# Performance work log

Measured on AMD Instinct MI355X. Metric: run time of the kernel, lower is better.

The kernel has to match this reference:

```python
import jax, jax.numpy as jnp
import numpy as np

EPS = 1e-5

def _layernorm(x, gamma, beta):
    mu = jnp.mean(x, axis=-1, keepdims=True)
    var = jnp.mean(jnp.square(x - mu), axis=-1, keepdims=True)
    return (x - mu) * jax.lax.rsqrt(var + EPS) * gamma + beta

def setup_inputs() -> dict:
    key = jax.random.key(0)
    ks = jax.random.split(key, 8)
    B, T, H = 8, 4096, 512
    s = 1.0 / np.sqrt(H)  # torch LSTM init scale
    return {
        "x": jax.random.normal(ks[0], (B, T, H), jnp.float32),
        "W_ih": jax.random.uniform(ks[1], (4 * H, H), jnp.float32, -s, s),
        "W_hh": jax.random.uniform(ks[2], (4 * H, H), jnp.float32, -s, s),
        "b_ih": jax.random.uniform(ks[3], (4 * H,), jnp.float32, -s, s),
        "b_hh": jax.random.uniform(ks[4], (4 * H,), jnp.float32, -s, s),
        "gamma": jnp.ones((H,), jnp.float32),
        "beta": jnp.zeros((H,), jnp.float32),
        "W_lin": jax.random.uniform(ks[5], (H, H), jnp.float32, -s, s),
        "b_lin": jax.random.uniform(ks[6], (H,), jnp.float32, -s, s),
    }

def _lstm(res, W_ih, W_hh, b_ih, b_hh):
    # res: [B, T, H]; torch gate order: i, f, g, o
    B, T, H = res.shape
    # precompute input contributions for all timesteps: [T, B, 4H]
    x_proj = jnp.einsum('bth,gh->tbg', res, W_ih) + (b_ih + b_hh)

    def step(carry, xp):
        h, c = carry  # [B, H] each
        gates = xp + h @ W_hh.T  # [B, 4H]
        i, f, g, o = jnp.split(gates, 4, axis=-1)
        i = jax.nn.sigmoid(i)
        f = jax.nn.sigmoid(f)
        g = jnp.tanh(g)
        o = jax.nn.sigmoid(o)
        c = f * c + i * g
        h = o * jnp.tanh(c)
        return (h, c), h

    h0 = jnp.zeros((B, H), res.dtype)
    c0 = jnp.zeros((B, H), res.dtype)
    (hT, cT), hs = jax.lax.scan(step, (h0, c0), x_proj)
    out = jnp.transpose(hs, (1, 0, 2))  # [B, T, H]
    return out, (hT[None], cT[None])

def reference(x, W_ih, W_hh, b_ih, b_hh, gamma, beta, W_lin, b_lin):
    res = _layernorm(x, gamma, beta)
    out, out_state = _lstm(res, W_ih, W_hh, b_ih, b_hh)
    gate = jax.nn.silu(res @ W_lin.T + b_lin)
    out = out * gate + res
    return (out, out_state)
```

## Files before the change

### kernel.cpp

```cpp
#include <hip/hip_runtime.h>
#include <math.h>

#define NB 8
#define HID 512

typedef unsigned int uint4v __attribute__((ext_vector_type(4)));

__device__ __forceinline__ float sigf(float x) { return 1.0f / (1.0f + __expf(-x)); }
__device__ __forceinline__ float tanhf_(float x) {
    return 2.0f / (1.0f + __expf(-2.0f * x)) - 1.0f;
}

__global__ void init_ws_kernel(unsigned long long* h_bufs) {
    h_bufs[blockIdx.x * 256 + threadIdx.x] = 0ull;
}

__global__ void ln_kernel(const float* __restrict__ x, const float* __restrict__ gamma,
                          const float* __restrict__ beta, float* __restrict__ res,
                          int t0, int chsh) {
    int wid = threadIdx.x >> 6, lane = threadIdx.x & 63;
    int rl = blockIdx.x * 4 + wid;
    int b = rl >> chsh, i = rl & ((1 << chsh) - 1);
    const float* xr = x + (long long)(b * 4096 + t0 + i) * HID;
    float4 u0 = *(const float4*)(xr + lane * 4);
    float4 u1 = *(const float4*)(xr + 256 + lane * 4);
    float s = u0.x + u0.y + u0.z + u0.w + u1.x + u1.y + u1.z + u1.w;
#pragma unroll
    for (int m = 1; m < 64; m <<= 1) s += __shfl_xor(s, m, 64);
    float mu = s * (1.0f / 512.0f);
    float d[8] = {u0.x - mu, u0.y - mu, u0.z - mu, u0.w - mu,
                  u1.x - mu, u1.y - mu, u1.z - mu, u1.w - mu};
    float q = d[0]*d[0] + d[1]*d[1] + d[2]*d[2] + d[3]*d[3] +
              d[4]*d[4] + d[5]*d[5] + d[6]*d[6] + d[7]*d[7];
#pragma unroll
    for (int m = 1; m < 64; m <<= 1) q += __shfl_xor(q, m, 64);
    float rs = rsqrtf(q * (1.0f / 512.0f) + 1e-5f);
    float4 g0 = *(const float4*)(gamma + lane * 4);
    float4 g1 = *(const float4*)(gamma + 256 + lane * 4);
    float4 b0 = *(const float4*)(beta + lane * 4);
    float4 b1 = *(const float4*)(beta + 256 + lane * 4);
    float* rr = res + (long long)rl * HID;
    float4 o0, o1;
    o0.x = d[0] * rs * g0.x + b0.x; o0.y = d[1] * rs * g0.y + b0.y;
    o0.z = d[2] * rs * g0.z + b0.z; o0.w = d[3] * rs * g0.w + b0.w;
    o1.x = d[4] * rs * g1.x + b1.x; o1.y = d[5] * rs * g1.y + b1.y;
    o1.z = d[6] * rs * g1.z + b1.z; o1.w = d[7] * rs * g1.w + b1.w;
    *(float4*)(rr + lane * 4) = o0;
    *(float4*)(rr + 256 + lane * 4) = o1;
}

template <int MODE>
__launch_bounds__(256, 2)
__global__ void gemm_nt(const float* __restrict__ A, const float* __restrict__ B,
                        const float* __restrict__ bias1, const float* __restrict__ bias2,
                        float* __restrict__ C, int N) {
    __shared__ float As[16][132];
    __shared__ float Bs[16][132];
    int tid = threadIdx.x;
    int tx = tid & 15, ty = tid >> 4;
    int r0 = blockIdx.x * 128;
    int j0 = blockIdx.y * 128;
    int arow = tid >> 2, ac = (tid & 3) * 4;

    float acc[8][8] = {};

    for (int kt = 0; kt < 512; kt += 16) {
        float4 a0 = *(const float4*)(A + (long long)(r0 + arow) * 512 + kt + ac);
        float4 a1 = *(const float4*)(A + (long long)(r0 + arow + 64) * 512 + kt + ac);
        float4 b0 = *(const float4*)(B + (long long)(j0 + arow) * 512 + kt + ac);
        float4 b1 = *(const float4*)(B + (long long)(j0 + arow + 64) * 512 + kt + ac);
        __syncthreads();
        As[ac + 0][arow] = a0.x; As[ac + 1][arow] = a0.y;
        As[ac + 2][arow] = a0.z; As[ac + 3][arow] = a0.w;
        As[ac + 0][arow + 64] = a1.x; As[ac + 1][arow + 64] = a1.y;
        As[ac + 2][arow + 64] = a1.z; As[ac + 3][arow + 64] = a1.w;
        Bs[ac + 0][arow] = b0.x; Bs[ac + 1][arow] = b0.y;
        Bs[ac + 2][arow] = b0.z; Bs[ac + 3][arow] = b0.w;
        Bs[ac + 0][arow + 64] = b1.x; Bs[ac + 1][arow + 64] = b1.y;
        Bs[ac + 2][arow + 64] = b1.z; Bs[ac + 3][arow + 64] = b1.w;
        __syncthreads();
#pragma unroll
        for (int kk = 0; kk < 16; kk++) {
            float a[8], bb[8];
            *(float4*)(a)      = *(const float4*)&As[kk][ty * 8];
            *(float4*)(a + 4)  = *(const float4*)&As[kk][ty * 8 + 4];
            *(float4*)(bb)     = *(const float4*)&Bs[kk][tx * 8];
            *(float4*)(bb + 4) = *(const float4*)&Bs[kk][tx * 8 + 4];
#pragma unroll
            for (int i = 0; i < 8; i++)
#pragma unroll
                for (int j = 0; j < 8; j++) acc[i][j] += a[i] * bb[j];
        }
    }

    float bv[8];
#pragma unroll
    for (int jj = 0; jj < 8; jj++) {
        int j = j0 + tx * 8 + jj;
        bv[jj] = (MODE == 0) ? (bias1[j] + bias2[j]) : bias1[j];
    }
#pragma unroll
    for (int ii = 0; ii < 8; ii++) {
        long long r = r0 + ty * 8 + ii;
        float* crow = C + r * (long long)N + j0 + tx * 8;
        float v[8];
#pragma unroll
        for (int jj = 0; jj < 8; jj++) {
            float tv = acc[ii][jj] + bv[jj];
            if (MODE == 1) tv = tv * sigf(tv);
            v[jj] = tv;
        }
        float4 o0, o1;
        o0.x = v[0]; o0.y = v[1]; o0.z = v[2]; o0.w = v[3];
        o1.x = v[4]; o1.y = v[5]; o1.z = v[6]; o1.w = v[7];
        *(float4*)(crow) = o0;
        *(float4*)(crow + 4) = o1;
    }
}

__launch_bounds__(256, 1)
__global__ void scan_kernel(const float* __restrict__ W_hh,
                            const float* __restrict__ xp,
                            const float* __restrict__ resv,
                            const float* __restrict__ gatev,
                            float* __restrict__ out,
                            unsigned long long* __restrict__ h_fast,
                            unsigned long long* __restrict__ h_safe,
                            float* __restrict__ c_buf,
                            int t0, int chsh) {
    const int CH = 1 << chsh;
    int b = blockIdx.x & 7, w = blockIdx.x >> 3;
    int tid = threadIdx.x;
    int kg = tid & 15, rq = tid >> 4;
    int slot = w * 16 + rq;

    __shared__ __align__(16) float lds[13312];

    const int ep_s = tid >> 2;
    const int ep_g = tid & 3;
    const int gr_s = tid & 63;

    float wreg[4][32];
#pragma unroll
    for (int g = 0; g < 4; g++) {
        const float* wr = W_hh + (long long)((g << 9) + slot) * 512 + (kg << 5);
#pragma unroll
        for (int q = 0; q < 8; q++) {
            float4 u = *(const float4*)(wr + q * 4);
            wreg[g][q * 4 + 0] = u.x; wreg[g][q * 4 + 1] = u.y;
            wreg[g][q * 4 + 2] = u.z; wreg[g][q * 4 + 3] = u.w;
        }
    }

    float c_reg = 0.0f;
    if (t0 > 0 && kg == 0) c_reg = c_buf[(b << 9) + slot];

    int mode = 0;
    const int pr0 = 2 * tid;
    const int n_w  = tid >> 1;
    const int pg_w = (n_w & ~7) | ((n_w ^ (n_w >> 3)) & 7);
    const int fi_w = (pg_w << 2) | (pr0 & 3);

    uint4v pa = {0, 0, 0, 0}, pb = {0, 0, 0, 0};
    float4 pfx0 = {0,0,0,0}, pfx1 = {0,0,0,0}, pfx2 = {0,0,0,0}, pfx3 = {0,0,0,0};
    float4 pfg0 = {0,0,0,0}, pfg1 = {0,0,0,0}, pfg2 = {0,0,0,0}, pfg3 = {0,0,0,0};

    {
        int row = (b << chsh) + ((ep_s < CH) ? ep_s : CH - 1);
        const float* xr = xp + (long long)row * 2048 + (ep_g << 9) + (w << 4);
        pfx0 = *(const float4*)(xr + 0);  pfx1 = *(const float4*)(xr + 4);
        pfx2 = *(const float4*)(xr + 8);  pfx3 = *(const float4*)(xr + 12);
        if (tid < 128) {
            int row2 = (b << chsh) + gr_s;
            const float* gr = (tid < 64 ? gatev : resv) + (long long)row2 * 512 + (w << 4);
            pfg0 = *(const float4*)(gr + 0);  pfg1 = *(const float4*)(gr + 4);
            pfg2 = *(const float4*)(gr + 8);  pfg3 = *(const float4*)(gr + 12);
        }
        asm volatile("s_waitcnt vmcnt(0)" ::: "memory");
        float* xd = lds + 1024 + (ep_s << 6) + (ep_g << 4);
        *(float4*)(xd + 0) = pfx0;  *(float4*)(xd + 4) = pfx1;
        *(float4*)(xd + 8) = pfx2;  *(float4*)(xd + 12) = pfx3;
        if (tid < 128) {
            float* gd = lds + (tid < 64 ? 9216 : 11264) + (gr_s << 4);
            *(float4*)(gd + 0) = pfg0;  *(float4*)(gd + 4) = pfg1;
            *(float4*)(gd + 8) = pfg2;  *(float4*)(gd + 12) = pfg3;
        }
    }

    for (int i = 0; i < CH; i++) {
        int t = t0 + i;
        int es = i & 63;
        int e = (i >> 6) & 1;
        int p = t & 1;

        float h0 = 0.0f, h1 = 0.0f;
        if (t > 0) {
            const int par = (t - 1) & 1;
            const unsigned exp_tag = (unsigned)t;
            bool got = false;
            if (mode == 0) {
                const unsigned long long* fb = h_fast + par * 4096 + (b << 9) + pr0;
                int tries = 0;
                asm volatile("global_load_dwordx4 %0, %1, off nt"
                             : "=v"(pa) : "v"(fb) : "memory");
                while (true) {
                    asm volatile("global_load_dwordx4 %0, %1, off nt"
                                 : "=v"(pb) : "v"(fb) : "memory");
                    asm volatile("s_waitcnt vmcnt(1)" : "+v"(pa) :: "memory");
                    if (pa[1] == exp_tag && pa[3] == exp_tag) {
                        h0 = __uint_as_float(pa[0]); h1 = __uint_as_float(pa[2]);
                        got = true; break;
                    }
                    asm volatile("global_load_dwordx4 %0, %1, off nt"
                                 : "=v"(pa) : "v"(fb) : "memory");
                    asm volatile("s_waitcnt vmcnt(1)" : "+v"(pb) :: "memory");
                    if (pb[1] == exp_tag && pb[3] == exp_tag) {
                        h0 = __uint_as_float(pb[0]); h1 = __uint_as_float(pb[2]);
                        got = true; break;
                    }
                    if (++tries > 512) { mode = 1; break; }
                }
            }
            if (!got) {
                const unsigned long long* sb = h_safe + par * 4096 + (b << 9);
                unsigned long long v0 = 0, v1 = 0;
                if (mode == 1) {
                    bool g0 = false, g1 = false;
                    int tr = 0;
                    while (true) {
                        if (!g0) {
                            v0 = __hip_atomic_load(sb + pr0, __ATOMIC_RELAXED,
                                                   __HIP_MEMORY_SCOPE_AGENT);
                            g0 = ((unsigned)(v0 >> 32) == exp_tag);
                        }
                        if (!g1) {
                            v1 = __hip_atomic_load(sb + pr0 + 1, __ATOMIC_RELAXED,
                                                   __HIP_MEMORY_SCOPE_AGENT);
                            g1 = ((unsigned)(v1 >> 32) == exp_tag);
                        }
                        if (g0 && g1) break;
                        if (++tr > (1 << 15)) { mode = 2; break; }
                    }
                } else {
                    v0 = __hip_atomic_load(sb + pr0, __ATOMIC_RELAXED,
                                           __HIP_MEMORY_SCOPE_AGENT);
                    v1 = __hip_atomic_load(sb + pr0 + 1, __ATOMIC_RELAXED,
                                           __HIP_MEMORY_SCOPE_AGENT);
                }
                h0 = __uint_as_float((unsigned)v0);
                h1 = __uint_as_float((unsigned)v1);
            }
            *(float2*)&lds[(p << 9) + fi_w] = make_float2(h0, h1);
        }

        if (es == 0) {
            int ib = i + 64;
            int sx = ib + ep_s; if (sx > CH - 1) sx = CH - 1;
            const float* xr = xp + (long long)((b << chsh) + sx) * 2048 + (ep_g << 9) + (w << 4);
            pfx0 = *(const float4*)(xr + 0);  pfx1 = *(const float4*)(xr + 4);
            pfx2 = *(const float4*)(xr + 8);  pfx3 = *(const float4*)(xr + 12);
            if (tid < 128) {
                int sy = ib + gr_s; if (sy > CH - 1) sy = CH - 1;
                const float* gr = (tid < 64 ? gatev : resv) + (long long)((b << chsh) + sy) * 512 + (w << 4);
                pfg0 = *(const float4*)(gr + 0);  pfg1 = *(const float4*)(gr + 4);
                pfg2 = *(const float4*)(gr + 8);  pfg3 = *(const float4*)(gr + 12);
            }
        }
        if (es == 1) {
            asm volatile("s_waitcnt vmcnt(0)" ::: "memory");
            int eo = e ^ 1;
            float* xd = lds + 1024 + (eo << 12) + (ep_s << 6) + (ep_g << 4);
            *(float4*)(xd + 0) = pfx0;  *(float4*)(xd + 4) = pfx1;
            *(float4*)(xd + 8) = pfx2;  *(float4*)(xd + 12) = pfx3;
            if (tid < 128) {
                float* gd = lds + (tid < 64 ? 9216 : 11264) + (eo << 10) + (gr_s << 4);
                *(float4*)(gd + 0) = pfg0;  *(float4*)(gd + 4) = pfg1;
                *(float4*)(gd + 8) = pfg2;  *(float4*)(gd + 12) = pfg3;
            }
        }

        asm volatile("s_waitcnt lgkmcnt(0)" ::: "memory");
        __builtin_amdgcn_s_barrier();
        asm volatile("" ::: "memory");

        float acc0 = 0, acc1 = 0, acc2 = 0, acc3 = 0;
        if (t > 0) {
            float hv[32];
#pragma unroll
            for (int q = 0; q < 8; q++) {
                int pg = (kg << 3) + (q ^ (kg & 7));
                float4 u = *(const float4*)&lds[(p << 9) + (pg << 2)];
                hv[q * 4 + 0] = u.x; hv[q * 4 + 1] = u.y;
                hv[q * 4 + 2] = u.z; hv[q * 4 + 3] = u.w;
            }
#pragma unroll
            for (int j = 0; j < 32; j++) {
                acc0 += hv[j] * wreg[0][j];
                acc1 += hv[j] * wreg[1][j];
                acc2 += hv[j] * wreg[2][j];
                acc3 += hv[j] * wreg[3][j];
            }
            acc0 += __shfl_xor(acc0, 1, 64); acc0 += __shfl_xor(acc0, 2, 64);
            acc0 += __shfl_xor(acc0, 4, 64); acc0 += __shfl_xor(acc0, 8, 64);
            acc1 += __shfl_xor(acc1, 1, 64); acc1 += __shfl_xor(acc1, 2, 64);
            acc1 += __shfl_xor(acc1, 4, 64); acc1 += __shfl_xor(acc1, 8, 64);
            acc2 += __shfl_xor(acc2, 1, 64); acc2 += __shfl_xor(acc2, 2, 64);
            acc2 += __shfl_xor(acc2, 4, 64); acc2 += __shfl_xor(acc2, 8, 64);
            acc3 += __shfl_xor(acc3, 1, 64); acc3 += __shfl_xor(acc3, 2, 64);
            acc3 += __shfl_xor(acc3, 4, 64); acc3 += __shfl_xor(acc3, 8, 64);
        }

        if (kg == 0) {
            const float* eb = lds + 1024 + (e << 12) + (es << 6);
            float xpv0 = eb[rq];
            float xpv1 = eb[16 + rq];
            float xpv2 = eb[32 + rq];
            float xpv3 = eb[48 + rq];
            float gv = lds[9216 + (e << 10) + (es << 4) + rq];
            float rv = lds[11264 + (e << 10) + (es << 4) + rq];
            float iv = sigf(acc0 + xpv0);
            float fv = sigf(acc1 + xpv1);
            float gt = tanhf_(acc2 + xpv2);
            float ov = sigf(acc3 + xpv3);
            c_reg = fv * c_reg + iv * gt;
            float h = ov * tanhf_(c_reg);
            unsigned long long pkt =
                ((unsigned long long)(unsigned)(t + 1) << 32) |
                (unsigned long long)__float_as_uint(h);
            __hip_atomic_store(h_safe + p * 4096 + (b << 9) + slot, pkt,
                               __ATOMIC_RELAXED, __HIP_MEMORY_SCOPE_AGENT);
            unsigned long long* fp = h_fast + p * 4096 + (b << 9) + slot;
            asm volatile("global_store_dwordx2 %0, %1, off sc0"
                         :: "v"(fp), "v"(pkt) : "memory");
            out[(long long)((b << 12) + t) * 512 + slot] = h * gv + rv;
            if (t == 4095) {
                out[16777216 + (b << 9) + slot] = h;
                out[16777216 + 4096 + (b << 9) + slot] = c_reg;
            }
            if (i == CH - 1) c_buf[(b << 9) + slot] = c_reg;
        }
    }
    asm volatile("s_waitcnt vmcnt(0)" :: "v"(pa), "v"(pb) : "memory");
}

extern "C" void kernel_launch(void* const* d_in, const int* in_sizes, int n_in,
                              void* d_out, int out_size, void* d_ws, size_t ws_size,
                              hipStream_t stream) {
    const float* x     = (const float*)d_in[0];
    const float* W_ih  = (const float*)d_in[1];
    const float* W_hh  = (const float*)d_in[2];
    const float* b_ih  = (const float*)d_in[3];
    const float* b_hh  = (const float*)d_in[4];
    const float* gamma = (const float*)d_in[5];
    const float* beta  = (const float*)d_in[6];
    const float* W_lin = (const float*)d_in[7];
    const float* b_lin = (const float*)d_in[8];
    float* out = (float*)d_out;

    const size_t small_bytes = 16384ull * 8 + 4096ull * 4;
    int CH = 256;
    for (int cand = 4096; cand >= 256; cand >>= 1) {
        if ((size_t)98304 * cand + small_bytes <= ws_size) { CH = cand; break; }
    }
    int chsh = 31 - __builtin_clz(CH);

    float* ws      = (float*)d_ws;
    float* res_ch  = ws;
    float* gate_ch = res_ch + (size_t)8 * CH * 512;
    float* xp_ch   = gate_ch + (size_t)8 * CH * 512;
    unsigned long long* h_fast = (unsigned long long*)(xp_ch + (size_t)8 * CH * 2048);
    unsigned long long* h_safe = h_fast + 8192;
    float* c_buf   = (float*)(h_safe + 8192);

    init_ws_kernel<<<64, 256, 0, stream>>>(h_fast);

    int nchunks = 4096 / CH;
    for (int c = 0; c < nchunks; c++) {
        int t0 = c * CH;
        ln_kernel<<<8 * CH / 4, 256, 0, stream>>>(x, gamma, beta, res_ch, t0, chsh);
        gemm_nt<0><<<dim3(8 * CH / 128, 16), 256, 0, stream>>>(res_ch, W_ih, b_ih, b_hh,
                                                               xp_ch, 2048);
        gemm_nt<1><<<dim3(8 * CH / 128, 4), 256, 0, stream>>>(res_ch, W_lin, b_lin, b_lin,
                                                              gate_ch, 512);
        scan_kernel<<<256, 256, 0, stream>>>(W_hh, xp_ch, res_ch, gate_ch, out,
                                             h_fast, h_safe, c_buf, t0, chsh);
    }
}
```

Baseline: 6.702 ms.

## Use bf16 MFMA for input projection and gate GEMMs

Converts W_ih and W_lin to bf16 once per call and has the layernorm kernel also write a bf16 copy of the normalized activations. The FP32 SIMT tiled GEMMs are replaced with a 128x128 tile kernel using mfma_f32_16x16x32_bf16, cutting GEMM compute time ahead of the sequential scan. It trades input precision (bf16 operands, fp32 accumulate) for throughput and adds workspace for the bf16 buffers, which may shrink the chunk size.

```diff
diff --git a/kernel.cpp b/kernel.cpp
--- a/kernel.cpp
+++ b/kernel.cpp
@@ -5,18 +5,36 @@
 #define HID 512
 
 typedef unsigned int uint4v __attribute__((ext_vector_type(4)));
+typedef __attribute__((ext_vector_type(8))) short short8v;
+typedef __attribute__((ext_vector_type(4))) float f32x4;
 
 __device__ __forceinline__ float sigf(float x) { return 1.0f / (1.0f + __expf(-x)); }
 __device__ __forceinline__ float tanhf_(float x) {
     return 2.0f / (1.0f + __expf(-2.0f * x)) - 1.0f;
 }
+__device__ __forceinline__ unsigned short f2bf(float f) {
+    unsigned u = __float_as_uint(f);
+    return (unsigned short)((u + 0x7FFFu + ((u >> 16) & 1u)) >> 16);
+}
 
 __global__ void init_ws_kernel(unsigned long long* h_bufs) {
     h_bufs[blockIdx.x * 256 + threadIdx.x] = 0ull;
 }
 
+__global__ void cvt_bf16_kernel(const float* __restrict__ src,
+                                unsigned short* __restrict__ dst, int n4) {
+    int i = blockIdx.x * 256 + threadIdx.x;
+    if (i < n4) {
+        float4 v = *(const float4*)(src + i * 4);
+        unsigned lo = (unsigned)f2bf(v.x) | ((unsigned)f2bf(v.y) << 16);
+        unsigned hi = (unsigned)f2bf(v.z) | ((unsigned)f2bf(v.w) << 16);
+        *(uint2*)(dst + i * 4) = make_uint2(lo, hi);
+    }
+}
+
 __global__ void ln_kernel(const float* __restrict__ x, const float* __restrict__ gamma,
                           const float* __restrict__ beta, float* __restrict__ res,
+                          unsigned short* __restrict__ res_bf,
                           int t0, int chsh) {
     int wid = threadIdx.x >> 6, lane = threadIdx.x & 63;
     int rl = blockIdx.x * 4 + wid;
@@ -47,74 +65,82 @@
     o1.z = d[6] * rs * g1.z + b1.z; o1.w = d[7] * rs * g1.w + b1.w;
     *(float4*)(rr + lane * 4) = o0;
     *(float4*)(rr + 256 + lane * 4) = o1;
+    unsigned short* rb = res_bf + (long long)rl * HID;
+    *(uint2*)(rb + lane * 4) = make_uint2(
+        (unsigned)f2bf(o0.x) | ((unsigned)f2bf(o0.y) << 16),
+        (unsigned)f2bf(o0.z) | ((unsigned)f2bf(o0.w) << 16));
+    *(uint2*)(rb + 256 + lane * 4) = make_uint2(
+        (unsigned)f2bf(o1.x) | ((unsigned)f2bf(o1.y) << 16),
+        (unsigned)f2bf(o1.z) | ((unsigned)f2bf(o1.w) << 16));
 }
 
 template <int MODE>
 __launch_bounds__(256, 2)
-__global__ void gemm_nt(const float* __restrict__ A, const float* __restrict__ B,
-                        const float* __restrict__ bias1, const float* __restrict__ bias2,
-                        float* __restrict__ C, int N) {
-    __shared__ float As[16][132];
-    __shared__ float Bs[16][132];
+__global__ void gemm_mfma(const unsigned short* __restrict__ A,
+                          const unsigned short* __restrict__ B,
+                          const float* __restrict__ bias1, const float* __restrict__ bias2,
+                          float* __restrict__ C, int N) {
+    __shared__ unsigned short Al[128][72];
+    __shared__ unsigned short Bl[128][72];
     int tid = threadIdx.x;
-    int tx = tid & 15, ty = tid >> 4;
-    int r0 = blockIdx.x * 128;
-    int j0 = blockIdx.y * 128;
-    int arow = tid >> 2, ac = (tid & 3) * 4;
-
-    float acc[8][8] = {};
-
-    for (int kt = 0; kt < 512; kt += 16) {
-        float4 a0 = *(const float4*)(A + (long long)(r0 + arow) * 512 + kt + ac);
-        float4 a1 = *(const float4*)(A + (long long)(r0 + arow + 64) * 512 + kt + ac);
-        float4 b0 = *(const float4*)(B + (long long)(j0 + arow) * 512 + kt + ac);
-        float4 b1 = *(const float4*)(B + (long long)(j0 + arow + 64) * 512 + kt + ac);
+    int lane = tid & 63, wv = tid >> 6;
+    int wr = wv >> 1, wc = wv & 1;
+    int r0 = blockIdx.x * 128, j0 = blockIdx.y * 128;
+    int srow = tid & 127, scol = (tid >> 7) * 32;
+
+    f32x4 acc[4][4];
+#pragma unroll
+    for (int m = 0; m < 4; m++)
+#pragma unroll
+        for (int n = 0; n < 4; n++) acc[m][n] = (f32x4){0.f, 0.f, 0.f, 0.f};
+
+    for (int kt = 0; kt < 512; kt += 64) {
+        const unsigned short* ag = A + (long long)(r0 + srow) * 512 + kt + scol;
+        const unsigned short* bg = B + (long long)(j0 + srow) * 512 + kt + scol;
+        float4 av0 = ((const float4*)ag)[0], av1 = ((const float4*)ag)[1],
+               av2 = ((const float4*)ag)[2], av3 = ((const float4*)ag)[3];
+        float4 bv0 = ((const float4*)bg)[0], bv1 = ((const float4*)bg)[1],
+               bv2 = ((const float4*)bg)[2], bv3 = ((const float4*)bg)[3];
         __syncthreads();
-        As[ac + 0][arow] = a0.x; As[ac + 1][arow] = a0.y;
-        As[ac + 2][arow] = a0.z; As[ac + 3][arow] = a0.w;
-        As[ac + 0][arow + 64] = a1.x; As[ac + 1][arow + 64] = a1.y;
-        As[ac + 2][arow + 64] = a1.z; As[ac + 3][arow + 64] = a1.w;
-        Bs[ac + 0][arow] = b0.x; Bs[ac + 1][arow] = b0.y;
-        Bs[ac + 2][arow] = b0.z; Bs[ac + 3][arow] = b0.w;
-        Bs[ac + 0][arow + 64] = b1.x; Bs[ac + 1][arow + 64] = b1.y;
-        Bs[ac + 2][arow + 64] = b1.z; Bs[ac + 3][arow + 64] = b1.w;
+        float4* ad = (float4*)&Al[srow][scol];
+        ad[0] = av0; ad[1] = av1; ad[2] = av2; ad[3] = av3;
+        float4* bd = (float4*)&Bl[srow][scol];
+        bd[0] = bv0; bd[1] = bv1; bd[2] = bv2; bd[3] = bv3;
         __syncthreads();
 #pragma unroll
-        for (int kk = 0; kk < 16; kk++) {
-            float a[8], bb[8];
-            *(float4*)(a)      = *(const float4*)&As[kk][ty * 8];
-            *(float4*)(a + 4)  = *(const float4*)&As[kk][ty * 8 + 4];
-            *(float4*)(bb)     = *(const float4*)&Bs[kk][tx * 8];
-            *(float4*)(bb + 4) = *(const float4*)&Bs[kk][tx * 8 + 4];
-#pragma unroll
-            for (int i = 0; i < 8; i++)
-#pragma unroll
-                for (int j = 0; j < 8; j++) acc[i][j] += a[i] * bb[j];
-        }
-    }
-
-    float bv[8];
-#pragma unroll
-    for (int jj = 0; jj < 8; jj++) {
-        int j = j0 + tx * 8 + jj;
-        bv[jj] = (MODE == 0) ? (bias1[j] + bias2[j]) : bias1[j];
-    }
-#pragma unroll
-    for (int ii = 0; ii < 8; ii++) {
-        long long r = r0 + ty * 8 + ii;
-        float* crow = C + r * (long long)N + j0 + tx * 8;
-        float v[8];
-#pragma unroll
-        for (int jj = 0; jj < 8; jj++) {
-            float tv = acc[ii][jj] + bv[jj];
-            if (MODE == 1) tv = tv * sigf(tv);
-            v[jj] = tv;
-        }
-        float4 o0, o1;
-        o0.x = v[0]; o0.y = v[1]; o0.z = v[2]; o0.w = v[3];
-        o1.x = v[4]; o1.y = v[5]; o1.z = v[6]; o1.w = v[7];
-        *(float4*)(crow) = o0;
-        *(float4*)(crow + 4) = o1;
+        for (int kk = 0; kk < 2; kk++) {
+            int krow = kk * 32 + ((lane >> 4) << 3);
+            short8v af[4], bf[4];
+#pragma unroll
+            for (int m = 0; m < 4; m++)
+                af[m] = *(const short8v*)&Al[wr * 64 + m * 16 + (lane & 15)][krow];
+#pragma unroll
+            for (int n = 0; n < 4; n++)
+                bf[n] = *(const short8v*)&Bl[wc * 64 + n * 16 + (lane & 15)][krow];
+#pragma unroll
+            for (int m = 0; m < 4; m++)
+#pragma unroll
+                for (int n = 0; n < 4; n++)
+                    acc[m][n] = __builtin_amdgcn_mfma_f32_16x16x32_bf16(
+                        af[m], bf[n], acc[m][n], 0, 0, 0);
+        }
+    }
+
+    int cl = lane & 15, rl4 = (lane >> 4) << 2;
+#pragma unroll
+    for (int n = 0; n < 4; n++) {
+        int j = j0 + wc * 64 + n * 16 + cl;
+        float bb = (MODE == 0) ? (bias1[j] + bias2[j]) : bias1[j];
+#pragma unroll
+        for (int m = 0; m < 4; m++) {
+#pragma unroll
+            for (int reg = 0; reg < 4; reg++) {
+                long long r = r0 + wr * 64 + m * 16 + rl4 + reg;
+                float tv = acc[m][n][reg] + bb;
+                if (MODE == 1) tv = tv * sigf(tv);
+                C[r * (long long)N + j] = tv;
+            }
+        }
     }
 }
 
@@ -357,10 +383,11 @@
     const float* b_lin = (const float*)d_in[8];
     float* out = (float*)d_out;
 
-    const size_t small_bytes = 16384ull * 8 + 4096ull * 4;
+    const size_t small_bytes = 16384ull * 8 + 4096ull * 4 +
+                               (2048ull * 512 + 512ull * 512) * 2;
     int CH = 256;
     for (int cand = 4096; cand >= 256; cand >>= 1) {
-        if ((size_t)98304 * cand + small_bytes <= ws_size) { CH = cand; break; }
+        if ((size_t)106496 * cand + small_bytes <= ws_size) { CH = cand; break; }
     }
     int chsh = 31 - __builtin_clz(CH);
 
@@ -368,20 +395,26 @@
     float* res_ch  = ws;
     float* gate_ch = res_ch + (size_t)8 * CH * 512;
     float* xp_ch   = gate_ch + (size_t)8 * CH * 512;
-    unsigned long long* h_fast = (unsigned long long*)(xp_ch + (size_t)8 * CH * 2048);
+    unsigned short* res_bf = (unsigned short*)(xp_ch + (size_t)8 * CH * 2048);
+    unsigned long long* h_fast = (unsigned long long*)(res_bf + (size_t)8 * CH * 512);
     unsigned long long* h_safe = h_fast + 8192;
     float* c_buf   = (float*)(h_safe + 8192);
+    unsigned short* wbf_ih  = (unsigned short*)(c_buf + 4096);
+    unsigned short* wbf_lin = wbf_ih + 2048 * 512;
 
     init_ws_kernel<<<64, 256, 0, stream>>>(h_fast);
+    cvt_bf16_kernel<<<1024, 256, 0, stream>>>(W_ih, wbf_ih, 2048 * 512 / 4);
+    cvt_bf16_kernel<<<256, 256, 0, stream>>>(W_lin, wbf_lin, 512 * 512 / 4);
 
     int nchunks = 4096 / CH;
     for (int c = 0; c < nchunks; c++) {
         int t0 = c * CH;
-        ln_kernel<<<8 * CH / 4, 256, 0, stream>>>(x, gamma, beta, res_ch, t0, chsh);
-        gemm_nt<0><<<dim3(8 * CH / 128, 16), 256, 0, stream>>>(res_ch, W_ih, b_ih, b_hh,
-                                                               xp_ch, 2048);
-        gemm_nt<1><<<dim3(8 * CH / 128, 4), 256, 0, stream>>>(res_ch, W_lin, b_lin, b_lin,
-                                                              gate_ch, 512);
+        ln_kernel<<<8 * CH / 4, 256, 0, stream>>>(x, gamma, beta, res_ch, res_bf,
+                                                  t0, chsh);
+        gemm_mfma<0><<<dim3(8 * CH / 128, 16), 256, 0, stream>>>(
+            res_bf, wbf_ih, b_ih, b_hh, xp_ch, 2048);
+        gemm_mfma<1><<<dim3(8 * CH / 128, 4), 256, 0, stream>>>(
+            res_bf, wbf_lin, b_lin, b_lin, gate_ch, 512);
         scan_kernel<<<256, 256, 0, stream>>>(W_hh, xp_ch, res_ch, gate_ch, out,
                                              h_fast, h_safe, c_buf, t0, chsh);
     }
```

Result: faster. 5.926 ms (median of 2 runs) (-11.6%).
